# Optimization experiments

Measured on AMD Instinct MI355X. Metric: run time of the kernel, lower is better.

The kernel has to match this reference:

```python
import jax, jax.numpy as jnp
import numpy as np

N = 100000   # nodes
E = 1600000  # directed edges (avg degree 16)
D = 128      # num_feature == hidden_channels


def setup_inputs() -> dict:
    key = jax.random.key(0)
    ks = jax.random.split(key, 8)
    s = 1.0 / np.sqrt(D)
    x = jax.random.normal(ks[0], (N, D), jnp.float32)
    edge_index = jax.random.randint(ks[1], (2, E), 0, N, dtype=jnp.int32)
    W1 = jax.random.normal(ks[2], (D, D), jnp.float32) * s
    W2 = jax.random.normal(ks[3], (D, D), jnp.float32) * s
    W3 = jax.random.normal(ks[4], (D, D), jnp.float32) * s
    b1 = jnp.zeros((D,), jnp.float32)
    b2 = jnp.zeros((D,), jnp.float32)
    b3 = jnp.zeros((D,), jnp.float32)
    return {"x": x, "edge_index": edge_index, "W1": W1, "b1": b1,
            "W2": W2, "b2": b2, "W3": W3, "b3": b3}


def reference(x, edge_index, W1, b1, W2, b2, W3, b3):
    # GCNConv with added self-loops and symmetric normalization:
    #   out = D^{-1/2} (A + I) D^{-1/2} (x W) + b
    loops = jnp.arange(N, dtype=edge_index.dtype)
    src = jnp.concatenate([edge_index[0], loops])  # [E+N]
    dst = jnp.concatenate([edge_index[1], loops])
    deg = jax.ops.segment_sum(jnp.ones_like(dst, x.dtype), dst, num_segments=N)
    dinv = jax.lax.rsqrt(deg)                      # deg >= 1 (self-loops)
    norm = dinv[src] * dinv[dst]                   # [E+N]

    def conv(h, W, b):
        h = h @ W                                   # [N, D] dense GEMM
        msg = h[src] * norm[:, None]                # gather + scale [E+N, D]
        return jax.ops.segment_sum(msg, dst, num_segments=N) + b

    # dropout is identity in eval mode
    h = jax.nn.relu(conv(x, W1, b1))
    h = jax.nn.relu(conv(h, W2, b2))
    return conv(h, W3, b3)
```

## Files before the change

kernel.cpp:

```cpp
#include <hip/hip_runtime.h>
#include <hip/hip_fp16.h>

#define DFEAT 128
#define BNODES 256
#define BSHIFT 8
#define B1CHUNK 2048
#define SLABC 8192

typedef _Float16 f16x8 __attribute__((ext_vector_type(8)));
typedef _Float16 f16x4 __attribute__((ext_vector_type(4)));
typedef float f32x4 __attribute__((ext_vector_type(4)));

__global__ __launch_bounds__(256) void bin_k(const int* __restrict__ src, const int* __restrict__ dst,
                                             int* __restrict__ gcnt, unsigned int* __restrict__ slab,
                                             int E, int nbuck) {
    __shared__ int cnt[512];
    __shared__ int off[512];
    __shared__ int gbase[512];
    __shared__ int sd[256];
    __shared__ unsigned int buf[B1CHUNK];
    __shared__ unsigned short bid[B1CHUNK];
    int t = threadIdx.x;
    int base = blockIdx.x * B1CHUNK;
    int nloc = E - base;
    if (nloc > B1CHUNK) nloc = B1CHUNK;
    cnt[t] = 0;
    cnt[t + 256] = 0;
    __syncthreads();
    for (int k = t; k < nloc; k += 256)
        atomicAdd(&cnt[dst[base + k] >> BSHIFT], 1);
    __syncthreads();
    int v0 = cnt[2 * t], v1 = cnt[2 * t + 1];
    int tsum = v0 + v1;
    sd[t] = tsum;
    __syncthreads();
    for (int o = 1; o < 256; o <<= 1) {
        int x = (t >= o) ? sd[t - o] : 0;
        __syncthreads();
        sd[t] += x;
        __syncthreads();
    }
    int texcl = sd[t] - tsum;
    off[2 * t] = texcl;
    off[2 * t + 1] = texcl + v0;
    if (2 * t < nbuck && v0 > 0) gbase[2 * t] = atomicAdd(&gcnt[2 * t], v0);
    if (2 * t + 1 < nbuck && v1 > 0) gbase[2 * t + 1] = atomicAdd(&gcnt[2 * t + 1], v1);
    __syncthreads();
    for (int k = t; k < nloc; k += 256) {
        int d = dst[base + k];
        int s = src[base + k];
        int b = d >> BSHIFT;
        int r = atomicAdd(&off[b], 1);
        buf[r] = ((unsigned)s << BSHIFT) | (unsigned)(d & (BNODES - 1));
        bid[r] = (unsigned short)b;
    }
    __syncthreads();
    for (int k = t; k < nloc; k += 256) {
        int b = bid[k];
        int o0 = off[b] - cnt[b];
        int pos = gbase[b] + (k - o0);
        if (pos < SLABC) slab[(size_t)b * SLABC + pos] = buf[k];
    }
}

__global__ __launch_bounds__(256) void scanb_k(const int* __restrict__ gcnt, int* __restrict__ bb,
                                               int* __restrict__ rp, int nbuck, int N, int E) {
    __shared__ int sd[256];
    int t = threadIdx.x;
    int v0 = (2 * t < nbuck) ? gcnt[2 * t] : 0;
    int v1 = (2 * t + 1 < nbuck) ? gcnt[2 * t + 1] : 0;
    int tsum = v0 + v1;
    sd[t] = tsum;
    __syncthreads();
    for (int o = 1; o < 256; o <<= 1) {
        int x = (t >= o) ? sd[t - o] : 0;
        __syncthreads();
        sd[t] += x;
        __syncthreads();
    }
    int excl = sd[t] - tsum;
    bb[2 * t] = excl;
    bb[2 * t + 1] = excl + v0;
    if (t == 0) rp[N] = E;
}

__global__ __launch_bounds__(256) void bucketAB_k(const unsigned int* __restrict__ slab,
                                                  const int* __restrict__ gcnt,
                                                  const int* __restrict__ bb,
                                                  int* __restrict__ rp, float* __restrict__ dinv,
                                                  int* __restrict__ cols, int N) {
    __shared__ int cnt[256];
    __shared__ int cur[256];
    __shared__ int outb[SLABC];
    int t = threadIdx.x;
    int b = blockIdx.x;
    int n0 = b << BSHIFT;
    int nn = N - n0;
    if (nn > BNODES) nn = BNODES;
    int ne = gcnt[b];
    if (ne > SLABC) ne = SLABC;
    int base = bb[b];
    const unsigned int* sl = slab + (size_t)b * SLABC;
    cnt[t] = 0;
    __syncthreads();
    for (int k = t; k < ne; k += 256)
        atomicAdd(&cnt[sl[k] & (BNODES - 1)], 1);
    __syncthreads();
    int deg = cnt[t];
    for (int o = 1; o < 256; o <<= 1) {
        int x = (t >= o) ? cnt[t - o] : 0;
        __syncthreads();
        cnt[t] += x;
        __syncthreads();
    }
    int excl = cnt[t] - deg;
    if (t < nn) {
        rp[n0 + t] = base + excl;
        dinv[n0 + t] = rsqrtf((float)(deg + 1));
    }
    cur[t] = excl;
    __syncthreads();
    for (int k = t; k < ne; k += 256) {
        unsigned r = sl[k];
        int pos = atomicAdd(&cur[r & (BNODES - 1)], 1);
        outb[pos] = (int)(r >> BSHIFT);
    }
    __syncthreads();
    for (int k = t; k < ne; k += 256)
        cols[base + k] = outb[k];
}

__global__ __launch_bounds__(256) void packW_k(const float* __restrict__ W0, const float* __restrict__ W1,
                                               const float* __restrict__ W2, _Float16* __restrict__ wpk) {
    int idx = blockIdx.x * 256 + threadIdx.x;
    int layer = idx >> 14;
    int e = idx & 16383;
    int k = e >> 7;
    int nn = e & 127;
    const float* W = (layer == 0) ? W0 : ((layer == 1) ? W1 : W2);
    float v = W[k * DFEAT + nn];
    int kc = k >> 5, quad = (k >> 3) & 3, j = k & 7;
    int ct = nn >> 4;
    int pos = ((ct * 4 + kc) * 64 + quad * 16 + (nn & 15)) * 8 + j;
    wpk[(size_t)layer * 16384 + pos] = (_Float16)v;
}


__device__ inline f16x4 ld4cvt(const float* p) {
    float4 v = *(const float4*)p;
    f16x4 h = { (_Float16)v.x, (_Float16)v.y, (_Float16)v.z, (_Float16)v.w };
    return h;
}
__device__ inline f16x4 ld4cvt(const __half* p) {
    return *(const f16x4*)p;
}

template <typename TIN>
__global__ __launch_bounds__(256) void gemmP_k(const TIN* __restrict__ A, const _Float16* __restrict__ wfrag,
                                               const float* __restrict__ dinv, __half* __restrict__ C, int n) {
    __shared__ _Float16 al[8192];
    const int tid = threadIdx.x;
    const int row0 = blockIdx.x * 64;
#pragma unroll
    for (int pass = 0; pass < 8; ++pass) {
        int r  = pass * 8 + (tid >> 5);
        int k4 = (tid & 31) * 4;
        int gr = row0 + r;
        f16x4 hv = { (_Float16)0.f, (_Float16)0.f, (_Float16)0.f, (_Float16)0.f };
        if (gr < n) hv = ld4cvt(&A[(size_t)gr * DFEAT + k4]);
        int wv_ = r >> 4, m = r & 15;
        int kc = k4 >> 5, quad = (k4 >> 3) & 3, j0 = k4 & 7;
        int dst = ((wv_ * 4 + kc) * 64 + quad * 16 + m) * 8 + j0;
        *(f16x4*)&al[dst] = hv;
    }
    __syncthreads();

    const int wv_  = tid >> 6;
    const int lane = tid & 63;
    f16x8 af[4];
#pragma unroll
    for (int kc = 0; kc < 4; ++kc)
        af[kc] = *(f16x8*)&al[((wv_ * 4 + kc) * 64 + lane) * 8];
    f32x4 acc[8];
#pragma unroll
    for (int ct = 0; ct < 8; ++ct) acc[ct] = (f32x4){0.f, 0.f, 0.f, 0.f};
#pragma unroll
    for (int ct = 0; ct < 8; ++ct) {
#pragma unroll
        for (int kc = 0; kc < 4; ++kc) {
            f16x8 bf = *(const f16x8*)&wfrag[((size_t)(ct * 4 + kc) * 64 + lane) * 8];
            acc[ct] = __builtin_amdgcn_mfma_f32_16x16x32_f16(af[kc], bf, acc[ct], 0, 0, 0);
        }
    }
    const int quad = lane >> 4, cb = lane & 15;
    const int rbase = row0 + wv_ * 16 + quad * 4;
    float ds[4];
#pragma unroll
    for (int r = 0; r < 4; ++r)
        ds[r] = (rbase + r < n) ? dinv[rbase + r] : 0.f;
#pragma unroll
    for (int ct = 0; ct < 8; ++ct) {
#pragma unroll
        for (int r = 0; r < 4; ++r) {
            int gr = rbase + r;
            if (gr < n) C[(size_t)gr * DFEAT + ct * 16 + cb] = __float2half(acc[ct][r] * ds[r]);
        }
    }
}


__device__ inline void st2(float* p, float x, float y) {
    float2 o; o.x = x; o.y = y;
    *(float2*)p = o;
}
__device__ inline void st2(__half* p, float x, float y) {
    *(__half2*)p = __floats2half2_rn(x, y);
}

template <typename TOUT>
__global__ __launch_bounds__(256) void agg_k(const __half* __restrict__ T, const float* __restrict__ dinv,
                                             const int* __restrict__ rowptr, const int* __restrict__ cols,
                                             const float* __restrict__ bias,
                                             TOUT* __restrict__ out, int relu, int n) {
    int wid = (int)((blockIdx.x * (size_t)blockDim.x + threadIdx.x) >> 6);
    int lane = threadIdx.x & 63;
    if (wid >= n) return;
    int fb = lane * 2;
    float2 t0 = __half22float2(*(const __half2*)(T + (size_t)wid * DFEAT + fb));
    float ax = t0.x;
    float ay = t0.y;
    int s = rowptr[wid], e = rowptr[wid + 1];
    for (int p = s; p < e; ) {
        int take = e - p;
        if (take > 64) take = 64;
        int q = p + lane;
        if (q >= e) q = e - 1;
        int ci = cols[q];
        int j = 0;
        for (; j + 8 <= take; j += 8) {
            int c0 = __builtin_amdgcn_readlane(ci, j + 0);
            int c1 = __builtin_amdgcn_readlane(ci, j + 1);
            int c2 = __builtin_amdgcn_readlane(ci, j + 2);
            int c3 = __builtin_amdgcn_readlane(ci, j + 3);
            int c4 = __builtin_amdgcn_readlane(ci, j + 4);
            int c5 = __builtin_amdgcn_readlane(ci, j + 5);
            int c6 = __builtin_amdgcn_readlane(ci, j + 6);
            int c7 = __builtin_amdgcn_readlane(ci, j + 7);
            float2 v0 = __half22float2(*(const __half2*)(T + (size_t)c0 * DFEAT + fb));
            float2 v1 = __half22float2(*(const __half2*)(T + (size_t)c1 * DFEAT + fb));
            float2 v2 = __half22float2(*(const __half2*)(T + (size_t)c2 * DFEAT + fb));
            float2 v3 = __half22float2(*(const __half2*)(T + (size_t)c3 * DFEAT + fb));
            float2 v4 = __half22float2(*(const __half2*)(T + (size_t)c4 * DFEAT + fb));
            float2 v5 = __half22float2(*(const __half2*)(T + (size_t)c5 * DFEAT + fb));
            float2 v6 = __half22float2(*(const __half2*)(T + (size_t)c6 * DFEAT + fb));
            float2 v7 = __half22float2(*(const __half2*)(T + (size_t)c7 * DFEAT + fb));
            ax += v0.x; ay += v0.y;
            ax += v1.x; ay += v1.y;
            ax += v2.x; ay += v2.y;
            ax += v3.x; ay += v3.y;
            ax += v4.x; ay += v4.y;
            ax += v5.x; ay += v5.y;
            ax += v6.x; ay += v6.y;
            ax += v7.x; ay += v7.y;
        }
        for (; j < take; ++j) {
            int c = __builtin_amdgcn_readlane(ci, j);
            float2 v = __half22float2(*(const __half2*)(T + (size_t)c * DFEAT + fb));
            ax += v.x; ay += v.y;
        }
        p += take;
    }
    float dw = dinv[wid];
    float ox = dw * ax + bias[fb];
    float oy = dw * ay + bias[fb + 1];
    if (relu) { ox = fmaxf(ox, 0.f); oy = fmaxf(oy, 0.f); }
    st2(&out[(size_t)wid * DFEAT + fb], ox, oy);
}


extern "C" void kernel_launch(void* const* d_in, const int* in_sizes, int n_in,
                              void* d_out, int out_size, void* d_ws, size_t ws_size,
                              hipStream_t stream) {
    const float* x  = (const float*)d_in[0];
    const int*   ei = (const int*)d_in[1];
    const float* W1 = (const float*)d_in[2];
    const float* b1 = (const float*)d_in[3];
    const float* W2 = (const float*)d_in[4];
    const float* b2 = (const float*)d_in[5];
    const float* W3 = (const float*)d_in[6];
    const float* b3 = (const float*)d_in[7];
    float* out = (float*)d_out;

    const int N = in_sizes[0] / DFEAT;
    const int E = in_sizes[1] / 2;
    const int* srcp = ei;
    const int* dstp = ei + E;

    size_t off = 0;
    auto alloc = [&](size_t bytes) -> void* {
        void* p = (char*)d_ws + off;
        off += (bytes + 255) & ~(size_t)255;
        return p;
    };
    const int nbuck = (N + BNODES - 1) / BNODES;

    int*    gcnt = (int*)alloc(2048);
    int*    bb   = (int*)alloc(2048);
    int*    rp   = (int*)alloc((size_t)(N + 1) * 4);
    float*  dinv = (float*)alloc((size_t)N * 4);
    _Float16* wpk = (_Float16*)alloc((size_t)3 * 16384 * 2);
    unsigned int* slab = (unsigned int*)alloc((size_t)nbuck * SLABC * 4);
    int*    cols = (int*)alloc((size_t)E * 4);
    __half* bufA = (__half*)alloc((size_t)N * DFEAT * 2);
    __half* bufB = (__half*)alloc((size_t)N * DFEAT * 2);

    hipMemsetAsync(gcnt, 0, 2048, stream);
    bin_k<<<(E + B1CHUNK - 1) / B1CHUNK, 256, 0, stream>>>(srcp, dstp, gcnt, slab, E, nbuck);
    scanb_k<<<1, 256, 0, stream>>>(gcnt, bb, rp, nbuck, N, E);
    bucketAB_k<<<nbuck, 256, 0, stream>>>(slab, gcnt, bb, rp, dinv, cols, N);
    packW_k<<<192, 256, 0, stream>>>(W1, W2, W3, wpk);

    int gemmGrid = (N + 63) / 64;
    int aggGrid  = (int)(((size_t)N * 64 + 255) / 256);

    gemmP_k<float><<<gemmGrid, 256, 0, stream>>>(x, wpk, dinv, bufA, N);
    agg_k<__half><<<aggGrid, 256, 0, stream>>>(bufA, dinv, rp, cols, b1, bufB, 1, N);

    gemmP_k<__half><<<gemmGrid, 256, 0, stream>>>(bufB, wpk + 16384, dinv, bufA, N);
    agg_k<__half><<<aggGrid, 256, 0, stream>>>(bufA, dinv, rp, cols, b2, bufB, 1, N);

    gemmP_k<__half><<<gemmGrid, 256, 0, stream>>>(bufB, wpk + 32768, dinv, bufA, N);
    agg_k<float><<<aggGrid, 256, 0, stream>>>(bufA, dinv, rp, cols, b3, out, 0, N);
}
```

Measured before the change: 431.1 us.

## Permute feature layout for vector GEMM stores, fuse scan, multi-tile GEMM blocks

The GEMM epilogue now writes 8 contiguous halves per row using a permuted column order. Weights, biases and the final output are permuted to compensate for that order. The separate bucket-offset scan kernel is removed, and each bucket block computes its own base by reducing the preceding counts. Binning and bucket loops are unrolled by four, the bin chunk size is doubled, and each GEMM block now processes three row tiles with register prefetch of the next tile. In exchange, the final output is written with scattered scalar stores, and the in-block prefix reduction does redundant work.

```diff
diff --git a/kernel.cpp b/kernel.cpp
--- a/kernel.cpp
+++ b/kernel.cpp
@@ -4,12 +4,14 @@
 #define DFEAT 128
 #define BNODES 256
 #define BSHIFT 8
-#define B1CHUNK 2048
+#define B1CHUNK 4096
 #define SLABC 8192
+#define TPB_TILES 3
 
 typedef _Float16 f16x8 __attribute__((ext_vector_type(8)));
 typedef _Float16 f16x4 __attribute__((ext_vector_type(4)));
 typedef float f32x4 __attribute__((ext_vector_type(4)));
+
 
 __global__ __launch_bounds__(256) void bin_k(const int* __restrict__ src, const int* __restrict__ dst,
                                              int* __restrict__ gcnt, unsigned int* __restrict__ slab,
@@ -27,8 +29,15 @@
     cnt[t] = 0;
     cnt[t + 256] = 0;
     __syncthreads();
-    for (int k = t; k < nloc; k += 256)
-        atomicAdd(&cnt[dst[base + k] >> BSHIFT], 1);
+    int k = t;
+    for (; k + 768 < nloc; k += 1024) {
+        int d0 = dst[base + k], d1 = dst[base + k + 256], d2 = dst[base + k + 512], d3 = dst[base + k + 768];
+        atomicAdd(&cnt[d0 >> BSHIFT], 1);
+        atomicAdd(&cnt[d1 >> BSHIFT], 1);
+        atomicAdd(&cnt[d2 >> BSHIFT], 1);
+        atomicAdd(&cnt[d3 >> BSHIFT], 1);
+    }
+    for (; k < nloc; k += 256) atomicAdd(&cnt[dst[base + k] >> BSHIFT], 1);
     __syncthreads();
     int v0 = cnt[2 * t], v1 = cnt[2 * t + 1];
     int tsum = v0 + v1;
@@ -46,7 +55,17 @@
     if (2 * t < nbuck && v0 > 0) gbase[2 * t] = atomicAdd(&gcnt[2 * t], v0);
     if (2 * t + 1 < nbuck && v1 > 0) gbase[2 * t + 1] = atomicAdd(&gcnt[2 * t + 1], v1);
     __syncthreads();
-    for (int k = t; k < nloc; k += 256) {
+    k = t;
+    for (; k + 768 < nloc; k += 1024) {
+        int d0 = dst[base + k], d1 = dst[base + k + 256], d2 = dst[base + k + 512], d3 = dst[base + k + 768];
+        int s0 = src[base + k], s1 = src[base + k + 256], s2 = src[base + k + 512], s3 = src[base + k + 768];
+        int b0 = d0 >> BSHIFT, b1_ = d1 >> BSHIFT, b2_ = d2 >> BSHIFT, b3_ = d3 >> BSHIFT;
+        int r0 = atomicAdd(&off[b0], 1); buf[r0] = ((unsigned)s0 << BSHIFT) | (unsigned)(d0 & (BNODES - 1)); bid[r0] = (unsigned short)b0;
+        int r1 = atomicAdd(&off[b1_], 1); buf[r1] = ((unsigned)s1 << BSHIFT) | (unsigned)(d1 & (BNODES - 1)); bid[r1] = (unsigned short)b1_;
+        int r2 = atomicAdd(&off[b2_], 1); buf[r2] = ((unsigned)s2 << BSHIFT) | (unsigned)(d2 & (BNODES - 1)); bid[r2] = (unsigned short)b2_;
+        int r3 = atomicAdd(&off[b3_], 1); buf[r3] = ((unsigned)s3 << BSHIFT) | (unsigned)(d3 & (BNODES - 1)); bid[r3] = (unsigned short)b3_;
+    }
+    for (; k < nloc; k += 256) {
         int d = dst[base + k];
         int s = src[base + k];
         int b = d >> BSHIFT;
@@ -55,7 +74,18 @@
         bid[r] = (unsigned short)b;
     }
     __syncthreads();
-    for (int k = t; k < nloc; k += 256) {
+    k = t;
+    for (; k + 768 < nloc; k += 1024) {
+#pragma unroll
+        for (int u = 0; u < 4; ++u) {
+            int kk = k + u * 256;
+            int b = bid[kk];
+            int o0 = off[b] - cnt[b];
+            int pos = gbase[b] + (kk - o0);
+            if (pos < SLABC) slab[(size_t)b * SLABC + pos] = buf[kk];
+        }
+    }
+    for (; k < nloc; k += 256) {
         int b = bid[k];
         int o0 = off[b] - cnt[b];
         int pos = gbase[b] + (k - o0);
@@ -63,48 +93,41 @@
     }
 }
 
-__global__ __launch_bounds__(256) void scanb_k(const int* __restrict__ gcnt, int* __restrict__ bb,
-                                               int* __restrict__ rp, int nbuck, int N, int E) {
-    __shared__ int sd[256];
-    int t = threadIdx.x;
-    int v0 = (2 * t < nbuck) ? gcnt[2 * t] : 0;
-    int v1 = (2 * t + 1 < nbuck) ? gcnt[2 * t + 1] : 0;
-    int tsum = v0 + v1;
-    sd[t] = tsum;
-    __syncthreads();
-    for (int o = 1; o < 256; o <<= 1) {
-        int x = (t >= o) ? sd[t - o] : 0;
-        __syncthreads();
-        sd[t] += x;
-        __syncthreads();
-    }
-    int excl = sd[t] - tsum;
-    bb[2 * t] = excl;
-    bb[2 * t + 1] = excl + v0;
-    if (t == 0) rp[N] = E;
-}
-
 __global__ __launch_bounds__(256) void bucketAB_k(const unsigned int* __restrict__ slab,
                                                   const int* __restrict__ gcnt,
-                                                  const int* __restrict__ bb,
                                                   int* __restrict__ rp, float* __restrict__ dinv,
-                                                  int* __restrict__ cols, int N) {
+                                                  int* __restrict__ cols, int N, int nbuck) {
     __shared__ int cnt[256];
     __shared__ int cur[256];
+    __shared__ int psum[256];
     __shared__ int outb[SLABC];
     int t = threadIdx.x;
     int b = blockIdx.x;
     int n0 = b << BSHIFT;
     int nn = N - n0;
     if (nn > BNODES) nn = BNODES;
-    int ne = gcnt[b];
-    if (ne > SLABC) ne = SLABC;
-    int base = bb[b];
+    int ne_raw = gcnt[b];
+    int ne = ne_raw > SLABC ? SLABC : ne_raw;
     const unsigned int* sl = slab + (size_t)b * SLABC;
+    int part = 0;
+    for (int i = t; i < b; i += 256) part += gcnt[i];
+    psum[t] = part;
     cnt[t] = 0;
     __syncthreads();
-    for (int k = t; k < ne; k += 256)
-        atomicAdd(&cnt[sl[k] & (BNODES - 1)], 1);
+    for (int o = 128; o > 0; o >>= 1) {
+        if (t < o) psum[t] += psum[t + o];
+        __syncthreads();
+    }
+    int base = psum[0];
+    int k = t;
+    for (; k + 768 < ne; k += 1024) {
+        unsigned a0 = sl[k], a1 = sl[k + 256], a2 = sl[k + 512], a3 = sl[k + 768];
+        atomicAdd(&cnt[a0 & (BNODES - 1)], 1);
+        atomicAdd(&cnt[a1 & (BNODES - 1)], 1);
+        atomicAdd(&cnt[a2 & (BNODES - 1)], 1);
+        atomicAdd(&cnt[a3 & (BNODES - 1)], 1);
+    }
+    for (; k < ne; k += 256) atomicAdd(&cnt[sl[k] & (BNODES - 1)], 1);
     __syncthreads();
     int deg = cnt[t];
     for (int o = 1; o < 256; o <<= 1) {
@@ -118,114 +141,149 @@
         rp[n0 + t] = base + excl;
         dinv[n0 + t] = rsqrtf((float)(deg + 1));
     }
+    if (b == nbuck - 1 && t == 0) rp[N] = base + ne_raw;
     cur[t] = excl;
     __syncthreads();
-    for (int k = t; k < ne; k += 256) {
-        unsigned r = sl[k];
-        int pos = atomicAdd(&cur[r & (BNODES - 1)], 1);
-        outb[pos] = (int)(r >> BSHIFT);
-    }
-    __syncthreads();
-    for (int k = t; k < ne; k += 256)
-        cols[base + k] = outb[k];
+    k = t;
+    for (; k + 768 < ne; k += 1024) {
+        unsigned a0 = sl[k], a1 = sl[k + 256], a2 = sl[k + 512], a3 = sl[k + 768];
+        int p0 = atomicAdd(&cur[a0 & (BNODES - 1)], 1); outb[p0] = (int)(a0 >> BSHIFT);
+        int p1 = atomicAdd(&cur[a1 & (BNODES - 1)], 1); outb[p1] = (int)(a1 >> BSHIFT);
+        int p2 = atomicAdd(&cur[a2 & (BNODES - 1)], 1); outb[p2] = (int)(a2 >> BSHIFT);
+        int p3 = atomicAdd(&cur[a3 & (BNODES - 1)], 1); outb[p3] = (int)(a3 >> BSHIFT);
+    }
+    for (; k < ne; k += 256) {
+        unsigned a = sl[k];
+        int p = atomicAdd(&cur[a & (BNODES - 1)], 1);
+        outb[p] = (int)(a >> BSHIFT);
+    }
+    __syncthreads();
+    k = t;
+    for (; k + 768 < ne; k += 1024) {
+        int o0 = outb[k], o1 = outb[k + 256], o2 = outb[k + 512], o3 = outb[k + 768];
+        cols[base + k] = o0;
+        cols[base + k + 256] = o1;
+        cols[base + k + 512] = o2;
+        cols[base + k + 768] = o3;
+    }
+    for (; k < ne; k += 256) cols[base + k] = outb[k];
 }
 
 __global__ __launch_bounds__(256) void packW_k(const float* __restrict__ W0, const float* __restrict__ W1,
-                                               const float* __restrict__ W2, _Float16* __restrict__ wpk) {
+                                               const float* __restrict__ W2,
+                                               const float* __restrict__ b0, const float* __restrict__ b1,
+                                               const float* __restrict__ b2,
+                                               _Float16* __restrict__ wpk, float* __restrict__ bp) {
     int idx = blockIdx.x * 256 + threadIdx.x;
     int layer = idx >> 14;
     int e = idx & 16383;
     int k = e >> 7;
     int nn = e & 127;
     const float* W = (layer == 0) ? W0 : ((layer == 1) ? W1 : W2);
-    float v = W[k * DFEAT + nn];
+    int ksrc = (layer == 0) ? k : (((k & 7) << 4) | (k >> 3));
+    float v = W[ksrc * DFEAT + nn];
     int kc = k >> 5, quad = (k >> 3) & 3, j = k & 7;
     int ct = nn >> 4;
     int pos = ((ct * 4 + kc) * 64 + quad * 16 + (nn & 15)) * 8 + j;
     wpk[(size_t)layer * 16384 + pos] = (_Float16)v;
-}
-
-
-__device__ inline f16x4 ld4cvt(const float* p) {
-    float4 v = *(const float4*)p;
-    f16x4 h = { (_Float16)v.x, (_Float16)v.y, (_Float16)v.z, (_Float16)v.w };
-    return h;
-}
-__device__ inline f16x4 ld4cvt(const __half* p) {
-    return *(const f16x4*)p;
-}
+    if (idx < 384) {
+        int l = idx >> 7, p = idx & 127;
+        int c = ((p & 7) << 4) | (p >> 3);
+        const float* bb = (l == 0) ? b0 : ((l == 1) ? b1 : b2);
+        bp[l * 128 + p] = bb[c];
+    }
+}
+
+
+template <typename T> struct LoadV;
+template <> struct LoadV<float>  { using T = float4; };
+template <> struct LoadV<__half> { using T = f16x4; };
+
+__device__ inline void ldraw(float4& d, const float* p) { d = *(const float4*)p; }
+__device__ inline void ldraw(f16x4& d, const __half* p) { d = *(const f16x4*)p; }
+__device__ inline void zro(float4& d) { d = make_float4(0.f, 0.f, 0.f, 0.f); }
+__device__ inline void zro(f16x4& d) { d = f16x4{(_Float16)0.f, (_Float16)0.f, (_Float16)0.f, (_Float16)0.f}; }
+__device__ inline f16x4 cvt4(const float4& v) { return f16x4{(_Float16)v.x, (_Float16)v.y, (_Float16)v.z, (_Float16)v.w}; }
+__device__ inline f16x4 cvt4(const f16x4& v) { return v; }
 
 template <typename TIN>
 __global__ __launch_bounds__(256) void gemmP_k(const TIN* __restrict__ A, const _Float16* __restrict__ wfrag,
-                                               const float* __restrict__ dinv, __half* __restrict__ C, int n) {
+                                               const float* __restrict__ dinv, __half* __restrict__ C,
+                                               int n, int ntiles) {
     __shared__ _Float16 al[8192];
+    using LV = typename LoadV<TIN>::T;
     const int tid = threadIdx.x;
-    const int row0 = blockIdx.x * 64;
-#pragma unroll
-    for (int pass = 0; pass < 8; ++pass) {
-        int r  = pass * 8 + (tid >> 5);
-        int k4 = (tid & 31) * 4;
-        int gr = row0 + r;
-        f16x4 hv = { (_Float16)0.f, (_Float16)0.f, (_Float16)0.f, (_Float16)0.f };
-        if (gr < n) hv = ld4cvt(&A[(size_t)gr * DFEAT + k4]);
-        int wv_ = r >> 4, m = r & 15;
-        int kc = k4 >> 5, quad = (k4 >> 3) & 3, j0 = k4 & 7;
-        int dst = ((wv_ * 4 + kc) * 64 + quad * 16 + m) * 8 + j0;
-        *(f16x4*)&al[dst] = hv;
-    }
-    __syncthreads();
-
-    const int wv_  = tid >> 6;
+    const int wv_ = tid >> 6;
     const int lane = tid & 63;
-    f16x8 af[4];
-#pragma unroll
-    for (int kc = 0; kc < 4; ++kc)
-        af[kc] = *(f16x8*)&al[((wv_ * 4 + kc) * 64 + lane) * 8];
-    f32x4 acc[8];
-#pragma unroll
-    for (int ct = 0; ct < 8; ++ct) acc[ct] = (f32x4){0.f, 0.f, 0.f, 0.f};
-#pragma unroll
-    for (int ct = 0; ct < 8; ++ct) {
-#pragma unroll
-        for (int kc = 0; kc < 4; ++kc) {
-            f16x8 bf = *(const f16x8*)&wfrag[((size_t)(ct * 4 + kc) * 64 + lane) * 8];
-            acc[ct] = __builtin_amdgcn_mfma_f32_16x16x32_f16(af[kc], bf, acc[ct], 0, 0, 0);
-        }
-    }
-    const int quad = lane >> 4, cb = lane & 15;
-    const int rbase = row0 + wv_ * 16 + quad * 4;
-    float ds[4];
-#pragma unroll
-    for (int r = 0; r < 4; ++r)
-        ds[r] = (rbase + r < n) ? dinv[rbase + r] : 0.f;
-#pragma unroll
-    for (int ct = 0; ct < 8; ++ct) {
+    const int t0 = blockIdx.x * TPB_TILES;
+    const int rS = (tid >> 5);
+    const int k4 = (tid & 31) * 4;
+
+    LV pre[8];
+    {
+        int row0 = t0 * 64;
+#pragma unroll
+        for (int p = 0; p < 8; ++p) {
+            int gr = row0 + p * 8 + rS;
+            if (gr < n) ldraw(pre[p], &A[(size_t)gr * DFEAT + k4]); else zro(pre[p]);
+        }
+    }
+    for (int tt = 0; tt < TPB_TILES; ++tt) {
+        int tile = t0 + tt;
+        if (tile >= ntiles) break;
+        int row0 = tile * 64;
+#pragma unroll
+        for (int p = 0; p < 8; ++p) {
+            int r = p * 8 + rS;
+            int wv2 = r >> 4, m = r & 15;
+            int kc = k4 >> 5, quad = (k4 >> 3) & 3, j0 = k4 & 7;
+            int dst = ((wv2 * 4 + kc) * 64 + quad * 16 + m) * 8 + j0;
+            *(f16x4*)&al[dst] = cvt4(pre[p]);
+        }
+        __syncthreads();
+        if (tt + 1 < TPB_TILES && tile + 1 < ntiles) {
+            int nrow0 = (tile + 1) * 64;
+#pragma unroll
+            for (int p = 0; p < 8; ++p) {
+                int gr = nrow0 + p * 8 + rS;
+                if (gr < n) ldraw(pre[p], &A[(size_t)gr * DFEAT + k4]); else zro(pre[p]);
+            }
+        }
+        f16x8 af[4];
+#pragma unroll
+        for (int kc = 0; kc < 4; ++kc)
+            af[kc] = *(f16x8*)&al[((wv_ * 4 + kc) * 64 + lane) * 8];
+        f32x4 acc[8];
+#pragma unroll
+        for (int ct = 0; ct < 8; ++ct) acc[ct] = (f32x4){0.f, 0.f, 0.f, 0.f};
+#pragma unroll
+        for (int ct = 0; ct < 8; ++ct) {
+#pragma unroll
+            for (int kc = 0; kc < 4; ++kc) {
+                f16x8 bf = *(const f16x8*)&wfrag[((size_t)(ct * 4 + kc) * 64 + lane) * 8];
+                acc[ct] = __builtin_amdgcn_mfma_f32_16x16x32_f16(af[kc], bf, acc[ct], 0, 0, 0);
+            }
+        }
+        const int quad = lane >> 4, cb = lane & 15;
+        const int rbase = row0 + wv_ * 16 + quad * 4;
 #pragma unroll
         for (int r = 0; r < 4; ++r) {
             int gr = rbase + r;
-            if (gr < n) C[(size_t)gr * DFEAT + ct * 16 + cb] = __float2half(acc[ct][r] * ds[r]);
-        }
-    }
-}
-
-
-__device__ inline void st2(float* p, float x, float y) {
-    float2 o; o.x = x; o.y = y;
-    *(float2*)p = o;
-}
-__device__ inline void st2(__half* p, float x, float y) {
-    *(__half2*)p = __floats2half2_rn(x, y);
-}
-
-template <typename TOUT>
-__global__ __launch_bounds__(256) void agg_k(const __half* __restrict__ T, const float* __restrict__ dinv,
-                                             const int* __restrict__ rowptr, const int* __restrict__ cols,
-                                             const float* __restrict__ bias,
-                                             TOUT* __restrict__ out, int relu, int n) {
-    int wid = (int)((blockIdx.x * (size_t)blockDim.x + threadIdx.x) >> 6);
-    int lane = threadIdx.x & 63;
-    if (wid >= n) return;
-    int fb = lane * 2;
+            if (gr < n) {
+                float dr = dinv[gr];
+                f16x8 o;
+#pragma unroll
+                for (int ct = 0; ct < 8; ++ct) o[ct] = (_Float16)(acc[ct][r] * dr);
+                *(f16x8*)&C[(size_t)gr * DFEAT + cb * 8] = o;
+            }
+        }
+        __syncthreads();
+    }
+}
+
+
+__device__ inline float2 agg_row(const __half* __restrict__ T, const int* __restrict__ rowptr,
+                                 const int* __restrict__ cols, int wid, int lane, int fb) {
     float2 t0 = __half22float2(*(const __half2*)(T + (size_t)wid * DFEAT + fb));
     float ax = t0.x;
     float ay = t0.y;
@@ -270,11 +328,40 @@
         }
         p += take;
     }
+    return make_float2(ax, ay);
+}
+
+__global__ __launch_bounds__(256) void agg_k(const __half* __restrict__ T, const float* __restrict__ dinv,
+                                             const int* __restrict__ rowptr, const int* __restrict__ cols,
+                                             const float* __restrict__ biasp,
+                                             __half* __restrict__ out, int n) {
+    int wid = (int)((blockIdx.x * (size_t)blockDim.x + threadIdx.x) >> 6);
+    int lane = threadIdx.x & 63;
+    if (wid >= n) return;
+    int fb = lane * 2;
+    float2 a = agg_row(T, rowptr, cols, wid, lane, fb);
     float dw = dinv[wid];
-    float ox = dw * ax + bias[fb];
-    float oy = dw * ay + bias[fb + 1];
-    if (relu) { ox = fmaxf(ox, 0.f); oy = fmaxf(oy, 0.f); }
-    st2(&out[(size_t)wid * DFEAT + fb], ox, oy);
+    float ox = fmaxf(dw * a.x + biasp[fb], 0.f);
+    float oy = fmaxf(dw * a.y + biasp[fb + 1], 0.f);
+    *(__half2*)(out + (size_t)wid * DFEAT + fb) = __floats2half2_rn(ox, oy);
+}
+
+__global__ __launch_bounds__(256) void aggF_k(const __half* __restrict__ T, const float* __restrict__ dinv,
+                                              const int* __restrict__ rowptr, const int* __restrict__ cols,
+                                              const float* __restrict__ biasp,
+                                              float* __restrict__ out, int n) {
+    int wid = (int)((blockIdx.x * (size_t)blockDim.x + threadIdx.x) >> 6);
+    int lane = threadIdx.x & 63;
+    if (wid >= n) return;
+    int fb = lane * 2;
+    float2 a = agg_row(T, rowptr, cols, wid, lane, fb);
+    float dw = dinv[wid];
+    float ox = dw * a.x + biasp[fb];
+    float oy = dw * a.y + biasp[fb + 1];
+    int c0 = ((fb & 7) << 4) | (fb >> 3);
+    int c1 = (((fb + 1) & 7) << 4) | ((fb + 1) >> 3);
+    out[(size_t)wid * DFEAT + c0] = ox;
+    out[(size_t)wid * DFEAT + c1] = oy;
 }
 
 
@@ -305,30 +392,30 @@
     const int nbuck = (N + BNODES - 1) / BNODES;
 
     int*    gcnt = (int*)alloc(2048);
-    int*    bb   = (int*)alloc(2048);
     int*    rp   = (int*)alloc((size_t)(N + 1) * 4);
     float*  dinv = (float*)alloc((size_t)N * 4);
     _Float16* wpk = (_Float16*)alloc((size_t)3 * 16384 * 2);
+    float*  bp   = (float*)alloc(3 * 128 * 4);
     unsigned int* slab = (unsigned int*)alloc((size_t)nbuck * SLABC * 4);
     int*    cols = (int*)alloc((size_t)E * 4);
     __half* bufA = (__half*)alloc((size_t)N * DFEAT * 2);
     __half* bufB = (__half*)alloc((size_t)N * DFEAT * 2);
 
+    packW_k<<<192, 256, 0, stream>>>(W1, W2, W3, b1, b2, b3, wpk, bp);
     hipMemsetAsync(gcnt, 0, 2048, stream);
     bin_k<<<(E + B1CHUNK - 1) / B1CHUNK, 256, 0, stream>>>(srcp, dstp, gcnt, slab, E, nbuck);
-    scanb_k<<<1, 256, 0, stream>>>(gcnt, bb, rp, nbuck, N, E);
-    bucketAB_k<<<nbuck, 256, 0, stream>>>(slab, gcnt, bb, rp, dinv, cols, N);
-    packW_k<<<192, 256, 0, stream>>>(W1, W2, W3, wpk);
-
-    int gemmGrid = (N + 63) / 64;
+    bucketAB_k<<<nbuck, 256, 0, stream>>>(slab, gcnt, rp, dinv, cols, N, nbuck);
+
+    int ntiles = (N + 63) / 64;
+    int gemmGrid = (ntiles + TPB_TILES - 1) / TPB_TILES;
     int aggGrid  = (int)(((size_t)N * 64 + 255) / 256);
 
-    gemmP_k<float><<<gemmGrid, 256, 0, stream>>>(x, wpk, dinv, bufA, N);
-    agg_k<__half><<<aggGrid, 256, 0, stream>>>(bufA, dinv, rp, cols, b1, bufB, 1, N);
-
-    gemmP_k<__half><<<gemmGrid, 256, 0, stream>>>(bufB, wpk + 16384, dinv, bufA, N);
-    agg_k<__half><<<aggGrid, 256, 0, stream>>>(bufA, dinv, rp, cols, b2, bufB, 1, N);
-
-    gemmP_k<__half><<<gemmGrid, 256, 0, stream>>>(bufB, wpk + 32768, dinv, bufA, N);
-    agg_k<float><<<aggGrid, 256, 0, stream>>>(bufA, dinv, rp, cols, b3, out, 0, N);
-}
+    gemmP_k<float><<<gemmGrid, 256, 0, stream>>>(x, wpk, dinv, bufA, N, ntiles);
+    agg_k<<<aggGrid, 256, 0, stream>>>(bufA, dinv, rp, cols, bp, bufB, N);
+
+    gemmP_k<__half><<<gemmGrid, 256, 0, stream>>>(bufB, wpk + 16384, dinv, bufA, N, ntiles);
+    agg_k<<<aggGrid, 256, 0, stream>>>(bufA, dinv, rp, cols, bp + 128, bufB, N);
+
+    gemmP_k<__half><<<gemmGrid, 256, 0, stream>>>(bufB, wpk + 32768, dinv, bufA, N, ntiles);
+    aggF_k<<<aggGrid, 256, 0, stream>>>(bufA, dinv, rp, cols, bp + 256, out, N);
+}
```

Measured after the change: 403.7 us. -6.4%, faster.
